# Kernel tuning notes

Hardware: AMD Instinct MI355X
Metric: run time of the kernel (lower is better)

The kernel has to match this reference:

```python
import jax, jax.numpy as jnp
import numpy as np

B, L, DIN = 32, 512, 768
H, DH = 16, 48
DOUT = H * DH
NEG = 1e12


def setup_inputs() -> dict:
    key = jax.random.key(0)
    ks = jax.random.split(key, 8)
    lim = float(np.sqrt(6.0 / (DIN + DOUT)))  # xavier_uniform
    return {
        "Q_seq": jax.random.normal(ks[0], (B, L, DIN), jnp.float32),
        "K_seq": jax.random.normal(ks[1], (B, L, DIN), jnp.float32),
        "V_seq": jax.random.normal(ks[2], (B, L, DIN), jnp.float32),
        "WQ": jax.random.uniform(ks[3], (DIN, DOUT), jnp.float32, -lim, lim),
        "WK": jax.random.uniform(ks[4], (DIN, DOUT), jnp.float32, -lim, lim),
        "WV": jax.random.uniform(ks[5], (DIN, DOUT), jnp.float32, -lim, lim),
        "Q_len": jax.random.randint(ks[6], (B, 1), 0, L, jnp.int64),
        "V_len": jax.random.randint(ks[7], (B, 1), 0, L, jnp.int64),
    }


def reference(Q_seq, K_seq, V_seq, WQ, WK, WV, Q_len, V_len):
    b, l = Q_seq.shape[0], Q_seq.shape[1]
    # projections -> [B, H, L, DH]
    q = (Q_seq @ WQ).reshape(b, l, H, DH).transpose(0, 2, 1, 3)
    k = (K_seq @ WK).reshape(b, l, H, DH).transpose(0, 2, 1, 3)
    v = (V_seq @ WV).reshape(b, l, H, DH).transpose(0, 2, 1, 3)
    # scaled scores [B, H, Lq, Lk]
    A = jnp.einsum("bhqd,bhkd->bhqk", q, k) / jnp.sqrt(jnp.float32(DH))
    # key-length additive mask (original: scatter+cumsum == arange < len)
    mask_k = (jnp.arange(l) < V_len[:, 0][:, None]).astype(A.dtype)  # [B, Lk]
    A = A - (1.0 - mask_k)[:, None, None, :] * NEG
    # causal mask (mask_right=True): subtract on strictly upper triangle
    A = A - jnp.triu(jnp.ones((l, l), A.dtype), 1) * NEG
    A = jax.nn.softmax(A, axis=-1)
    # original quirk: O = A^T @ V  -> O[b,h,k,d] = sum_q A[b,h,q,k] V[b,h,q,d]
    O = jnp.einsum("bhqk,bhqd->bkhd", A, v).reshape(b, l, DOUT)
    # query-length multiplicative mask on output
    mask_q = (jnp.arange(l) < Q_len[:, 0][:, None]).astype(O.dtype)  # [B, L]
    return O * mask_q[:, :, None]
```

## Files before the change

kernel.cpp:

```cpp
#include <hip/hip_runtime.h>
#include <stdint.h>

#define B_    32
#define L_    512
#define DIN_  768
#define H_    16
#define DH_   48
#define DOUT_ 768
#define NHEADS (B_ * H_)
#define HEADELEMS (L_ * DH_)

typedef short bf16x8 __attribute__((ext_vector_type(8)));
typedef float f32x4  __attribute__((ext_vector_type(4)));

__device__ __forceinline__ uint16_t f2bf(float f) {
  uint32_t u = __float_as_uint(f);
  u += 0x7fffu + ((u >> 16) & 1u);
  return (uint16_t)(u >> 16);
}
__device__ __forceinline__ uint32_t pack2bf(float lo, float hi) {
  uint32_t a = __float_as_uint(lo);
  a += 0x7fffu + ((a >> 16) & 1u);
  uint32_t b = __float_as_uint(hi);
  b += 0x7fffu + ((b >> 16) & 1u);
  return (a >> 16) | (b & 0xffff0000u);
}
__device__ __forceinline__ void gload_lds16(const void* g, void* l) {
  __builtin_amdgcn_global_load_lds(
      (const __attribute__((address_space(1))) uint32_t*)g,
      (__attribute__((address_space(3))) uint32_t*)l, 16, 0, 0);
}
__device__ __forceinline__ bf16x8 lds_frag8(const uint16_t* p) {
  union { uint2 u[2]; bf16x8 v; } x;
  x.u[0] = *(const uint2*)(p);
  x.u[1] = *(const uint2*)(p + 4);
  return x.v;
}

__global__ void lens_kernel(const int* __restrict__ qlen_raw,
                            const int* __restrict__ vlen_raw,
                            int* __restrict__ lens) {
  __shared__ int is64[2];
  int t = threadIdx.x;
  if (t < 2) {
    const int* src = (t == 0) ? qlen_raw : vlen_raw;
    int o = 0;
    for (int i = 0; i < 16; ++i) o |= src[2 * i + 1];
    is64[t] = (o == 0) ? 1 : 0;
  }
  __syncthreads();
  int which = t >> 5;
  int i = t & 31;
  const int* src = which ? vlen_raw : qlen_raw;
  lens[t] = is64[which] ? src[2 * i] : src[i];
}

__global__ void wconv_kernel(const float* __restrict__ WQ,
                             const float* __restrict__ WK,
                             const float* __restrict__ WV,
                             uint16_t* __restrict__ Wt) {
  const int z = blockIdx.z;
  const float* W = (z == 0) ? WQ : (z == 1) ? WK : WV;
  const float sc = (z == 0) ? 0.14433756729740643f : 1.0f;
  uint16_t* dst = Wt + (size_t)z * DIN_ * DOUT_;
  const int n  = blockIdx.x * 256 + threadIdx.x;
  const int k4 = blockIdx.y * 4;
  float f0 = W[(size_t)(k4 + 0) * DOUT_ + n] * sc;
  float f1 = W[(size_t)(k4 + 1) * DOUT_ + n] * sc;
  float f2 = W[(size_t)(k4 + 2) * DOUT_ + n] * sc;
  float f3 = W[(size_t)(k4 + 3) * DOUT_ + n] * sc;
  uint2 p;
  p.x = pack2bf(f0, f1);
  p.y = pack2bf(f2, f3);
  *(uint2*)&dst[(size_t)n * DIN_ + k4] = p;
}

__global__ __launch_bounds__(512, 4) void mfma_proj(
    const float* __restrict__ Xq, const float* __restrict__ Xk,
    const float* __restrict__ Xv, const uint16_t* __restrict__ Wt,
    uint16_t* __restrict__ qh, uint16_t* __restrict__ kh,
    uint16_t* __restrict__ vh) {
  const int z = blockIdx.z;
  const float* X = (z == 0) ? Xq : (z == 1) ? Xk : Xv;
  uint16_t* dst  = (z == 0) ? qh : (z == 1) ? kh : vh;
  const uint16_t* W = Wt + (size_t)z * DIN_ * DOUT_;

  __shared__ uint16_t As[128][32];
  __shared__ uint16_t Bs[128][32];

  const int t  = threadIdx.x;
  const int m0 = blockIdx.x * 128;
  const int n0 = blockIdx.y * 128;

  const int csw = ((t & 3) ^ ((t >> 3) & 3)) * 8;

  const int ra = t >> 2;
  const float* aptr = X + (size_t)(m0 + ra) * DIN_ + csw;

  const uint16_t* bptr = W + (size_t)(n0 + (t >> 2)) * DIN_ + csw;
  void* ldsB = (char*)(&Bs[0][0]) + t * 16;
  void* ldsA = (char*)(&As[0][0]) + t * 16;

  const int w = t >> 6, lane = t & 63;
  const int wm = (w & 3) * 32, wn = (w >> 2) * 64;
  const int fr = lane & 15;
  const int quad = lane >> 4;

  f32x4 acc[2][4];
#pragma unroll
  for (int i = 0; i < 2; ++i)
#pragma unroll
    for (int j = 0; j < 4; ++j) acc[i][j] = f32x4{0.f, 0.f, 0.f, 0.f};

  for (int kt = 0; kt < DIN_ / 32; ++kt) {
    const int k0 = kt * 32;
    gload_lds16(bptr + k0, ldsB);
    float4 x0 = *(const float4*)(aptr + k0);
    float4 x1 = *(const float4*)(aptr + k0 + 4);
    uint4 pA;
    pA.x = pack2bf(x0.x, x0.y); pA.y = pack2bf(x0.z, x0.w);
    pA.z = pack2bf(x1.x, x1.y); pA.w = pack2bf(x1.z, x1.w);
    *(uint4*)ldsA = pA;
    __syncthreads();

    bf16x8 af[2], bfr[4];
#pragma unroll
    for (int i = 0; i < 2; ++i) {
      const int r = wm + i * 16 + fr;
      af[i]  = *(const bf16x8*)&As[r][(quad ^ ((r >> 1) & 3)) * 8];
    }
#pragma unroll
    for (int j = 0; j < 4; ++j) {
      const int r = wn + j * 16 + fr;
      bfr[j] = *(const bf16x8*)&Bs[r][(quad ^ ((r >> 1) & 3)) * 8];
    }
#pragma unroll
    for (int mt = 0; mt < 2; ++mt)
#pragma unroll
      for (int nt = 0; nt < 4; ++nt)
        acc[mt][nt] = __builtin_amdgcn_mfma_f32_16x16x32_bf16(
            af[mt], bfr[nt], acc[mt][nt], 0, 0, 0);
    __syncthreads();
  }

#pragma unroll
  for (int mt = 0; mt < 2; ++mt) {
#pragma unroll
    for (int r = 0; r < 4; ++r) {
      const int m  = m0 + wm + mt * 16 + quad * 4 + r;
      const int bb = m >> 9;
      const int l  = m & 511;
#pragma unroll
      for (int nt = 0; nt < 4; ++nt) {
        const int n = n0 + wn + nt * 16 + fr;
        const int h = n / DH_;
        const int d = n - h * DH_;
        dst[(((size_t)bb * H_ + h) * L_ + l) * DH_ + d] = f2bf(acc[mt][nt][r]);
      }
    }
  }
}

__global__ __launch_bounds__(256, 2) void attn_mfma(
    const uint16_t* __restrict__ qh, const uint16_t* __restrict__ kh,
    const uint16_t* __restrict__ vh, const int* __restrict__ lens,
    float* __restrict__ out) {
  const int bh = blockIdx.x;
  const int b  = bh >> 4;
  const int h  = bh & 15;
  const int t    = threadIdx.x;
  const int w    = t >> 6;
  const int lane = t & 63;
  const int l15  = lane & 15;
  const int quad = lane >> 4;

  const int qlen = lens[b];
  const int vlen = lens[32 + b];
  const bool deg = (vlen == 0);
  const size_t head = (size_t)bh * HEADELEMS;

  __shared__ uint16_t Pt[4][128][36];
  __shared__ uint16_t Vt[48][36];
  __shared__ float    prt[4][32];

  const uint16_t* qbase = qh + head;
  const uint16_t* kbase = kh + head;
  const uint16_t* vbase = vh + head;

  f32x4 Oacc[8][3];
#pragma unroll
  for (int i = 0; i < 8; ++i)
#pragma unroll
    for (int dt = 0; dt < 3; ++dt) Oacc[i][dt] = f32x4{0.f, 0.f, 0.f, 0.f};

  for (int g = 0; g < 16; ++g) {
    const int q0 = g * 32;
    const int lim = q0 + 31 - 16 * w;

    __syncthreads();

    if (t < 192) {
      const int vq = t & 31, oct = t >> 5;
      uint4 u = *(const uint4*)(vbase + (size_t)(q0 + vq) * DH_ + oct * 8);
      const int d0 = oct * 8;
      Vt[d0 + 0][vq] = (uint16_t)(u.x);
      Vt[d0 + 1][vq] = (uint16_t)(u.x >> 16);
      Vt[d0 + 2][vq] = (uint16_t)(u.y);
      Vt[d0 + 3][vq] = (uint16_t)(u.y >> 16);
      Vt[d0 + 4][vq] = (uint16_t)(u.z);
      Vt[d0 + 5][vq] = (uint16_t)(u.z >> 16);
      Vt[d0 + 6][vq] = (uint16_t)(u.w);
      Vt[d0 + 7][vq] = (uint16_t)(u.w >> 16);
    }

    bf16x8 aq[2][2];
#pragma unroll
    for (int mt = 0; mt < 2; ++mt) {
      const uint16_t* qp = qbase + (size_t)(q0 + mt * 16 + l15) * DH_;
      aq[mt][0] = *(const bf16x8*)(qp + quad * 8);
      bf16x8 zz = {0, 0, 0, 0, 0, 0, 0, 0};
      aq[mt][1] = zz;
      if (quad < 2) aq[mt][1] = *(const bf16x8*)(qp + 32 + quad * 8);
    }

    float lrun[2][4];
#pragma unroll
    for (int mt = 0; mt < 2; ++mt)
#pragma unroll
      for (int r = 0; r < 4; ++r) lrun[mt][r] = 0.0f;

#pragma unroll
    for (int i = 0; i < 8; ++i) {
      if (64 * i > lim) continue;
      const int kb = 64 * i + 16 * w;
      f32x4 s0 = {0.f, 0.f, 0.f, 0.f};
      f32x4 s1 = {0.f, 0.f, 0.f, 0.f};
      if (!deg) {
        const uint16_t* kp = kbase + (size_t)(kb + l15) * DH_;
        bf16x8 bk0 = *(const bf16x8*)(kp + quad * 8);
        bf16x8 bk1 = {0, 0, 0, 0, 0, 0, 0, 0};
        if (quad < 2) bk1 = *(const bf16x8*)(kp + 32 + quad * 8);
        s0 = __builtin_amdgcn_mfma_f32_16x16x32_bf16(aq[0][0], bk0, s0, 0, 0, 0);
        s0 = __builtin_amdgcn_mfma_f32_16x16x32_bf16(aq[0][1], bk1, s0, 0, 0, 0);
        s1 = __builtin_amdgcn_mfma_f32_16x16x32_bf16(aq[1][0], bk0, s1, 0, 0, 0);
        s1 = __builtin_amdgcn_mfma_f32_16x16x32_bf16(aq[1][1], bk1, s1, 0, 0, 0);
      }
      const int kc  = kb + l15;
      const int row = i * 16 + l15;
#pragma unroll
      for (int mt = 0; mt < 2; ++mt) {
        f32x4 sv = (mt == 0) ? s0 : s1;
        float p4[4];
#pragma unroll
        for (int r = 0; r < 4; ++r) {
          const int qrow = q0 + mt * 16 + quad * 4 + r;
          float e;
          if (deg) {
            e = (kc <= qrow) ? 1.0f : 0.0f;
          } else {
            e = (kc < vlen && kc <= qrow) ? __expf(sv[r]) : 0.0f;
          }
          lrun[mt][r] += e;
          p4[r] = e;
        }
        const int col = mt * 16 + quad * 4;
        *(uint32_t*)&Pt[w][row][col]     = pack2bf(p4[0], p4[1]);
        *(uint32_t*)&Pt[w][row][col + 2] = pack2bf(p4[2], p4[3]);
      }
    }

#pragma unroll
    for (int mt = 0; mt < 2; ++mt)
#pragma unroll
      for (int r = 0; r < 4; ++r) {
        float l = lrun[mt][r];
#pragma unroll
        for (int off = 1; off < 16; off <<= 1) l += __shfl_xor(l, off, 64);
        lrun[mt][r] = l;
      }
    if (l15 == 0) {
#pragma unroll
      for (int mt = 0; mt < 2; ++mt)
#pragma unroll
        for (int r = 0; r < 4; ++r)
          prt[w][mt * 16 + quad * 4 + r] = lrun[mt][r];
    }
    __syncthreads();

    {
      const int q = t & 31;
      const float inv = __builtin_amdgcn_rcpf(
          prt[0][q] + prt[1][q] + prt[2][q] + prt[3][q]);
#pragma unroll
      for (int j = 0; j < 6; ++j) {
        const int d = (t >> 5) + 8 * j;
        float f = __uint_as_float((uint32_t)Vt[d][q] << 16) * inv;
        Vt[d][q] = f2bf(f);
      }
    }
    __syncthreads();

    bf16x8 bv[3];
#pragma unroll
    for (int dt = 0; dt < 3; ++dt)
      bv[dt] = lds_frag8(&Vt[dt * 16 + l15][quad * 8]);
#pragma unroll
    for (int i = 0; i < 8; ++i) {
      if (64 * i > lim) continue;
      bf16x8 ap = lds_frag8(&Pt[w][i * 16 + l15][quad * 8]);
#pragma unroll
      for (int dt = 0; dt < 3; ++dt)
        Oacc[i][dt] = __builtin_amdgcn_mfma_f32_16x16x32_bf16(
            ap, bv[dt], Oacc[i][dt], 0, 0, 0);
    }
  }

#pragma unroll
  for (int i = 0; i < 8; ++i) {
#pragma unroll
    for (int r = 0; r < 4; ++r) {
      const int k_abs = 64 * i + 16 * w + quad * 4 + r;
      const float msk = (k_abs < qlen) ? 1.0f : 0.0f;
      float* orow = out + (size_t)(b * L_ + k_abs) * DOUT_ + h * DH_;
#pragma unroll
      for (int dt = 0; dt < 3; ++dt)
        orow[dt * 16 + l15] = Oacc[i][dt][r] * msk;
    }
  }
}

extern "C" void kernel_launch(void* const* d_in, const int* in_sizes, int n_in,
                              void* d_out, int out_size, void* d_ws, size_t ws_size,
                              hipStream_t stream) {
  const float* Qs  = (const float*)d_in[0];
  const float* Kse = (const float*)d_in[1];
  const float* Vs  = (const float*)d_in[2];
  const float* WQ  = (const float*)d_in[3];
  const float* WK  = (const float*)d_in[4];
  const float* WV  = (const float*)d_in[5];
  const int*   Qlen = (const int*)d_in[6];
  const int*   Vlen = (const int*)d_in[7];
  float* out = (float*)d_out;

  char* ws = (char*)d_ws;
  int* lens = (int*)ws;
  uint16_t* qh = (uint16_t*)(ws + 256);
  uint16_t* kh = qh + (size_t)B_ * H_ * L_ * DH_;
  uint16_t* vh = kh + (size_t)B_ * H_ * L_ * DH_;
  uint16_t* Wt = vh + (size_t)B_ * H_ * L_ * DH_;

  lens_kernel<<<1, 64, 0, stream>>>(Qlen, Vlen, lens);
  wconv_kernel<<<dim3(3, 192, 3), 256, 0, stream>>>(WQ, WK, WV, Wt);
  mfma_proj<<<dim3(16384 / 128, DOUT_ / 128, 3), 512, 0, stream>>>(
      Qs, Kse, Vs, Wt, qh, kh, vh);
  attn_mfma<<<NHEADS, 256, 0, stream>>>(qh, kh, vh, lens, out);
}
```

Before: 339.6 us.

## Pre-convert activations to bf16 and widen projection GEMM tile to 128x256

Adds a separate pass that converts the fp32 Q/K/V inputs to bf16 in workspace. The projection GEMM can then load A tiles directly into LDS with global_load_lds instead of converting fp32 in registers. The GEMM tile grows to 128x256, with each wave computing a 64x64 block, to reuse each loaded A tile across more MFMAs. The cost is an extra read and write of the activations in global memory, plus more accumulator registers per thread, which may lower occupancy.

```diff
diff --git a/kernel.cpp b/kernel.cpp
--- a/kernel.cpp
+++ b/kernel.cpp
@@ -9,6 +9,7 @@
 #define DOUT_ 768
 #define NHEADS (B_ * H_)
 #define HEADELEMS (L_ * DH_)
+#define MROWS (B_ * L_)
 
 typedef short bf16x8 __attribute__((ext_vector_type(8)));
 typedef float f32x4  __attribute__((ext_vector_type(4)));
@@ -75,57 +76,67 @@
   *(uint2*)&dst[(size_t)n * DIN_ + k4] = p;
 }
 
+__global__ void xconv_kernel(const float* __restrict__ Xq,
+                             const float* __restrict__ Xk,
+                             const float* __restrict__ Xv,
+                             uint16_t* __restrict__ Xbf) {
+  const int z = blockIdx.y;
+  const float* src = (z == 0) ? Xq : (z == 1) ? Xk : Xv;
+  uint16_t* dst = Xbf + (size_t)z * MROWS * DIN_;
+  const size_t i = ((size_t)blockIdx.x * 256 + threadIdx.x) * 8;
+  float4 x0 = *(const float4*)(src + i);
+  float4 x1 = *(const float4*)(src + i + 4);
+  uint4 p;
+  p.x = pack2bf(x0.x, x0.y); p.y = pack2bf(x0.z, x0.w);
+  p.z = pack2bf(x1.x, x1.y); p.w = pack2bf(x1.z, x1.w);
+  *(uint4*)(dst + i) = p;
+}
+
 __global__ __launch_bounds__(512, 4) void mfma_proj(
-    const float* __restrict__ Xq, const float* __restrict__ Xk,
-    const float* __restrict__ Xv, const uint16_t* __restrict__ Wt,
+    const uint16_t* __restrict__ Xbf, const uint16_t* __restrict__ Wt,
     uint16_t* __restrict__ qh, uint16_t* __restrict__ kh,
     uint16_t* __restrict__ vh) {
   const int z = blockIdx.z;
-  const float* X = (z == 0) ? Xq : (z == 1) ? Xk : Xv;
+  const uint16_t* X = Xbf + (size_t)z * MROWS * DIN_;
   uint16_t* dst  = (z == 0) ? qh : (z == 1) ? kh : vh;
   const uint16_t* W = Wt + (size_t)z * DIN_ * DOUT_;
 
   __shared__ uint16_t As[128][32];
-  __shared__ uint16_t Bs[128][32];
+  __shared__ uint16_t Bs[256][32];
 
   const int t  = threadIdx.x;
   const int m0 = blockIdx.x * 128;
-  const int n0 = blockIdx.y * 128;
+  const int n0 = blockIdx.y * 256;
 
   const int csw = ((t & 3) ^ ((t >> 3) & 3)) * 8;
-
-  const int ra = t >> 2;
-  const float* aptr = X + (size_t)(m0 + ra) * DIN_ + csw;
-
-  const uint16_t* bptr = W + (size_t)(n0 + (t >> 2)) * DIN_ + csw;
-  void* ldsB = (char*)(&Bs[0][0]) + t * 16;
-  void* ldsA = (char*)(&As[0][0]) + t * 16;
+  const uint16_t* aptr  = X + (size_t)(m0 + (t >> 2)) * DIN_ + csw;
+  const uint16_t* bptr0 = W + (size_t)(n0 + (t >> 2)) * DIN_ + csw;
+  const uint16_t* bptr1 = W + (size_t)(n0 + 128 + (t >> 2)) * DIN_ + csw;
+  void* ldsA  = (char*)(&As[0][0]) + t * 16;
+  void* ldsB0 = (char*)(&Bs[0][0]) + t * 16;
+  void* ldsB1 = (char*)(&Bs[0][0]) + (t + 512) * 16;
 
   const int w = t >> 6, lane = t & 63;
-  const int wm = (w & 3) * 32, wn = (w >> 2) * 64;
+  const int wm = (w & 1) * 64, wn = (w >> 1) * 64;
   const int fr = lane & 15;
   const int quad = lane >> 4;
 
-  f32x4 acc[2][4];
-#pragma unroll
-  for (int i = 0; i < 2; ++i)
+  f32x4 acc[4][4];
+#pragma unroll
+  for (int i = 0; i < 4; ++i)
 #pragma unroll
     for (int j = 0; j < 4; ++j) acc[i][j] = f32x4{0.f, 0.f, 0.f, 0.f};
 
   for (int kt = 0; kt < DIN_ / 32; ++kt) {
     const int k0 = kt * 32;
-    gload_lds16(bptr + k0, ldsB);
-    float4 x0 = *(const float4*)(aptr + k0);
-    float4 x1 = *(const float4*)(aptr + k0 + 4);
-    uint4 pA;
-    pA.x = pack2bf(x0.x, x0.y); pA.y = pack2bf(x0.z, x0.w);
-    pA.z = pack2bf(x1.x, x1.y); pA.w = pack2bf(x1.z, x1.w);
-    *(uint4*)ldsA = pA;
-    __syncthreads();
-
-    bf16x8 af[2], bfr[4];
-#pragma unroll
-    for (int i = 0; i < 2; ++i) {
+    gload_lds16(aptr + k0, ldsA);
+    gload_lds16(bptr0 + k0, ldsB0);
+    gload_lds16(bptr1 + k0, ldsB1);
+    __syncthreads();
+
+    bf16x8 af[4], bfr[4];
+#pragma unroll
+    for (int i = 0; i < 4; ++i) {
       const int r = wm + i * 16 + fr;
       af[i]  = *(const bf16x8*)&As[r][(quad ^ ((r >> 1) & 3)) * 8];
     }
@@ -135,7 +146,7 @@
       bfr[j] = *(const bf16x8*)&Bs[r][(quad ^ ((r >> 1) & 3)) * 8];
     }
 #pragma unroll
-    for (int mt = 0; mt < 2; ++mt)
+    for (int mt = 0; mt < 4; ++mt)
 #pragma unroll
       for (int nt = 0; nt < 4; ++nt)
         acc[mt][nt] = __builtin_amdgcn_mfma_f32_16x16x32_bf16(
@@ -144,7 +155,7 @@
   }
 
 #pragma unroll
-  for (int mt = 0; mt < 2; ++mt) {
+  for (int mt = 0; mt < 4; ++mt) {
 #pragma unroll
     for (int r = 0; r < 4; ++r) {
       const int m  = m0 + wm + mt * 16 + quad * 4 + r;
@@ -344,14 +355,16 @@
 
   char* ws = (char*)d_ws;
   int* lens = (int*)ws;
-  uint16_t* qh = (uint16_t*)(ws + 256);
-  uint16_t* kh = qh + (size_t)B_ * H_ * L_ * DH_;
-  uint16_t* vh = kh + (size_t)B_ * H_ * L_ * DH_;
-  uint16_t* Wt = vh + (size_t)B_ * H_ * L_ * DH_;
+  uint16_t* qh  = (uint16_t*)(ws + 256);
+  uint16_t* kh  = qh + (size_t)B_ * H_ * L_ * DH_;
+  uint16_t* vh  = kh + (size_t)B_ * H_ * L_ * DH_;
+  uint16_t* Wt  = vh + (size_t)B_ * H_ * L_ * DH_;
+  uint16_t* Xbf = Wt + (size_t)3 * DIN_ * DOUT_;
 
   lens_kernel<<<1, 64, 0, stream>>>(Qlen, Vlen, lens);
   wconv_kernel<<<dim3(3, 192, 3), 256, 0, stream>>>(WQ, WK, WV, Wt);
-  mfma_proj<<<dim3(16384 / 128, DOUT_ / 128, 3), 512, 0, stream>>>(
-      Qs, Kse, Vs, Wt, qh, kh, vh);
+  xconv_kernel<<<dim3(MROWS * DIN_ / 2048, 3), 256, 0, stream>>>(Qs, Kse, Vs, Xbf);
+  mfma_proj<<<dim3(MROWS / 128, DOUT_ / 256, 3), 512, 0, stream>>>(
+      Xbf, Wt, qh, kh, vh);
   attn_mfma<<<NHEADS, 256, 0, stream>>>(qh, kh, vh, lens, out);
 }
```

After: 343.5 us. No clear change (+1.1%).
